# Optimization experiments

Measured on AMD Instinct MI355X. Metric: run time of the kernel, lower is better.

Reference implementation:

```python
import jax, jax.numpy as jnp
import numpy as np

# dims
B, L, IN_SIZE = 8, 4096, 1024
D_MODEL = 256            # hidden_size1
D_INNER = 512            # expand * d_model
D_STATE = 16             # mamba-ssm default
D_CONV = 4               # mamba-ssm default
DT_RANK = 16             # ceil(d_model / 16)
NUM_CLASSES = 2


def setup_inputs() -> dict:
    key = jax.random.key(0)
    ks = jax.random.split(key, 14)
    rn = lambda k, shape, s=0.02: jax.random.normal(k, shape, jnp.float32) * s
    inp = {
        "x": jax.random.normal(ks[0], (B, L, IN_SIZE), jnp.float32),
        "fc1_w": rn(ks[1], (D_MODEL, IN_SIZE)),
        "fc1_b": jnp.zeros((D_MODEL,), jnp.float32),
        "in_proj_w": rn(ks[2], (2 * D_INNER, D_MODEL)),
        "conv_w": rn(ks[3], (D_INNER, D_CONV), 0.1),
        "conv_b": jnp.zeros((D_INNER,), jnp.float32),
        "x_proj_w": rn(ks[4], (DT_RANK + 2 * D_STATE, D_INNER)),
        "dt_proj_w": rn(ks[5], (D_INNER, DT_RANK), 0.1),
        "dt_proj_b": jax.random.uniform(ks[6], (D_INNER,), jnp.float32, -4.0, -2.0),
        "A_log": jnp.tile(jnp.log(jnp.arange(1, D_STATE + 1, dtype=jnp.float32)), (D_INNER, 1)),
        "D_skip": jnp.ones((D_INNER,), jnp.float32),
        "out_proj_w": rn(ks[7], (D_MODEL, D_INNER)),
        "fc3_w": rn(ks[8], (NUM_CLASSES, D_MODEL)),
        "fc3_b": jnp.zeros((NUM_CLASSES,), jnp.float32),
    }
    return inp


def _mamba(h, in_proj_w, conv_w, conv_b, x_proj_w, dt_proj_w, dt_proj_b, A_log, D_skip, out_proj_w):
    # h: (B, L, D_MODEL)
    xz = jnp.einsum('bld,ed->ble', h, in_proj_w)          # (B, L, 2*D_INNER)
    u, z = jnp.split(xz, 2, axis=-1)                      # (B, L, D_INNER) each

    # depthwise causal conv1d along L
    uc = jnp.swapaxes(u, 1, 2)                            # (B, D_INNER, L)
    kw = conv_w[:, None, :]                               # (D_INNER, 1, K)
    uc = jax.lax.conv_general_dilated(
        uc, kw, window_strides=(1,), padding=[(D_CONV - 1, 0)],
        feature_group_count=D_INNER, dimension_numbers=('NCH', 'OIH', 'NCH'))
    uc = jax.nn.silu(uc + conv_b[None, :, None])
    u = jnp.swapaxes(uc, 1, 2)                            # (B, L, D_INNER)

    x_dbl = jnp.einsum('bld,ed->ble', u, x_proj_w)        # (B, L, DT_RANK+2*D_STATE)
    dt = x_dbl[..., :DT_RANK]
    Bmat = x_dbl[..., DT_RANK:DT_RANK + D_STATE]          # (B, L, D_STATE)
    Cmat = x_dbl[..., DT_RANK + D_STATE:]                 # (B, L, D_STATE)
    dt = jax.nn.softplus(jnp.einsum('blr,dr->bld', dt, dt_proj_w) + dt_proj_b)

    A = -jnp.exp(A_log)                                   # (D_INNER, D_STATE)

    def step(hstate, inp):
        dt_t, B_t, C_t, u_t = inp                         # (B,D),(B,S),(B,S),(B,D)
        dA = jnp.exp(dt_t[:, :, None] * A)                # (B, D, S)
        hstate = dA * hstate + (dt_t * u_t)[:, :, None] * B_t[:, None, :]
        y_t = jnp.einsum('bds,bs->bd', hstate, C_t)
        return hstate, y_t

    xs = (jnp.swapaxes(dt, 0, 1), jnp.swapaxes(Bmat, 0, 1),
          jnp.swapaxes(Cmat, 0, 1), jnp.swapaxes(u, 0, 1))
    h0 = jnp.zeros((u.shape[0], D_INNER, D_STATE), u.dtype)
    _, ys = jax.lax.scan(step, h0, xs)                    # ys: (L, B, D_INNER)
    y = jnp.swapaxes(ys, 0, 1) + u * D_skip               # (B, L, D_INNER)
    y = y * jax.nn.silu(z)
    return jnp.einsum('bld,ed->ble', y, out_proj_w)       # (B, L, D_MODEL)


def reference(x, fc1_w, fc1_b, in_proj_w, conv_w, conv_b, x_proj_w,
              dt_proj_w, dt_proj_b, A_log, D_skip, out_proj_w, fc3_w, fc3_b):
    h = jax.nn.gelu(jnp.einsum('bli,hi->blh', x, fc1_w) + fc1_b, approximate=False)
    h = _mamba(h, in_proj_w, conv_w, conv_b, x_proj_w, dt_proj_w,
               dt_proj_b, A_log, D_skip, out_proj_w)
    pooled = h.mean(axis=1)                               # (B, D_MODEL)
    return pooled @ fc3_w.T + fc3_b                       # (B, NUM_CLASSES)
```

## Files before the change

kernel.cpp:

```cpp
#include <hip/hip_runtime.h>
#include <math.h>

#define BB 8
#define LL 4096
#define BL (BB*LL)
#define IN_SZ 1024
#define D_MODEL 256
#define D_INNER 512
#define D_STATE 16
#define DT_RANK 16
#define NCLS 2
#define NCHUNK 64
#define CLEN (LL/NCHUNK)

#define OFF_XB16  ((size_t)0)
#define OFF_HB    (OFF_XB16 + (size_t)BL*1024*2)
#define OFF_XZB   (OFF_HB   + (size_t)BL*256*2)
#define OFF_UCB   (OFF_XZB  + (size_t)BL*1024*2)
#define OFF_YB    (OFF_UCB  + (size_t)BL*512*2)
#define OFF_DT    (OFF_YB   + (size_t)BL*512*2)
#define OFF_XBC   (OFF_DT   + (size_t)BL*512*4)
#define OFF_HLOC  (OFF_XBC  + (size_t)BL*32*4)
#define OFF_PP    (OFF_HLOC + (size_t)BB*NCHUNK*16*512*4)
#define OFF_H2    (OFF_PP   + (size_t)BB*NCHUNK*16*512*4)
#define OFF_WCAT  (OFF_H2   + (size_t)BL*256*4)
#define OFF_FC1WB (OFF_WCAT + (size_t)544*512*2)
#define OFF_IPWB  (OFF_FC1WB+ (size_t)256*1024*2)
#define OFF_OPWB  (OFF_IPWB + (size_t)1024*256*2)
#define OFF_POOL  (OFF_OPWB + (size_t)256*512*2)

typedef __bf16 bf16x8 __attribute__((ext_vector_type(8)));
typedef float  f32x4  __attribute__((ext_vector_type(4)));

__device__ __forceinline__ unsigned short f2bf(float f) {
    union { float f; unsigned u; } v; v.f = f;
    unsigned r = (v.u + 0x7fffu + ((v.u >> 16) & 1u)) >> 16;
    return (unsigned short)r;
}
__device__ __forceinline__ int pack2(float lo, float hi) {
    return (int)((unsigned)f2bf(lo) | ((unsigned)f2bf(hi) << 16));
}
__device__ __forceinline__ float b2f(unsigned short u) {
    union { unsigned u; float f; } v; v.u = (unsigned)u << 16; return v.f;
}
__device__ __forceinline__ float fexp(float x) { return __expf(x); }

#define GLOAD16(g, l) __builtin_amdgcn_global_load_lds( \
    (const __attribute__((address_space(1))) void*)(g), \
    (__attribute__((address_space(3))) void*)(l), 16, 0, 0)

template<int EPI, bool BOUND, int OUTBF>
__global__ __launch_bounds__(256) void gemm_bf16(
    const unsigned short* __restrict__ A, int lda,
    const unsigned short* __restrict__ Bw, int ldb,
    void* __restrict__ Cout, int ldc,
    float* __restrict__ C2,
    const float* __restrict__ bias,
    int N, int K)
{
    __shared__ unsigned short smem[2 * 128 * 64];

    const int tid  = threadIdx.x;
    const int m0   = blockIdx.y * 128;
    const int n0   = blockIdx.x * 128;
    const int wv   = tid >> 6;
    const int lane = tid & 63;
    const int wr   = wv >> 1;
    const int wc   = wv & 1;
    const int r0   = lane & 15;
    const int kgf  = lane >> 4;

    f32x4 acc[4][4];
#pragma unroll
    for (int i = 0; i < 4; i++)
#pragma unroll
        for (int j = 0; j < 4; j++) acc[i][j] = (f32x4){0.f, 0.f, 0.f, 0.f};

    for (int k0 = 0; k0 < K; k0 += 64) {
        __syncthreads();
#pragma unroll
        for (int r = 0; r < 4; r++) {
            int q   = r * 4 + wv;
            int row = q * 8 + (lane >> 3);
            int c   = (lane & 7) ^ (row & 7);
            const unsigned short* ga = A + (size_t)(m0 + row) * lda + k0 + c * 8;
            GLOAD16(ga, &smem[q * 512]);
            int nn = n0 + row;
            if (BOUND && nn > N - 1) nn = N - 1;
            const unsigned short* gb = Bw + (size_t)nn * ldb + k0 + c * 8;
            GLOAD16(gb, &smem[8192 + q * 512]);
        }
        __syncthreads();

#pragma unroll
        for (int kk = 0; kk < 2; kk++) {
            bf16x8 af[4], bfq[4];
            const int sl = ((kk << 2) + kgf) ^ (r0 & 7);
#pragma unroll
            for (int mi = 0; mi < 4; mi++)
                af[mi] = *reinterpret_cast<const bf16x8*>(
                    &smem[(wr * 64 + mi * 16 + r0) * 64 + sl * 8]);
#pragma unroll
            for (int ni = 0; ni < 4; ni++)
                bfq[ni] = *reinterpret_cast<const bf16x8*>(
                    &smem[8192 + (wc * 64 + ni * 16 + r0) * 64 + sl * 8]);
#pragma unroll
            for (int mi = 0; mi < 4; mi++)
#pragma unroll
                for (int ni = 0; ni < 4; ni++)
                    acc[mi][ni] = __builtin_amdgcn_mfma_f32_16x16x32_bf16(
                        af[mi], bfq[ni], acc[mi][ni], 0, 0, 0);
        }
    }

#pragma unroll
    for (int mi = 0; mi < 4; mi++) {
#pragma unroll
        for (int ni = 0; ni < 4; ni++) {
            int col = n0 + wc * 64 + ni * 16 + r0;
            if (BOUND && col >= N) continue;
#pragma unroll
            for (int j = 0; j < 4; j++) {
                int row = m0 + wr * 64 + mi * 16 + kgf * 4 + j;
                float v = acc[mi][ni][j];
                if (EPI == 1) {
                    v += bias[col];
                    v = 0.5f * v * (1.0f + erff(v * 0.70710678118654752f));
                } else if (EPI == 2) {
                    v += bias[col];
                    v = fmaxf(v, 0.f) + log1pf(fexp(-fabsf(v)));
                }
                if (EPI == 3) {
                    if (col < 512) {
                        v += bias[col];
                        v = fmaxf(v, 0.f) + log1pf(fexp(-fabsf(v)));
                        ((float*)Cout)[(size_t)row * 512 + col] = v;
                    } else {
                        C2[(size_t)row * 32 + (col - 512)] = v;
                    }
                } else if (OUTBF) {
                    ((unsigned short*)Cout)[(size_t)row * ldc + col] = f2bf(v);
                } else {
                    ((float*)Cout)[(size_t)row * ldc + col] = v;
                }
            }
        }
    }
}

__global__ __launch_bounds__(256) void f2b_kernel(
    const float* __restrict__ src, unsigned short* __restrict__ dst, int n8)
{
    int i = blockIdx.x * 256 + threadIdx.x;
    if (i >= n8) return;
    const float4* s = reinterpret_cast<const float4*>(src) + (size_t)i * 2;
    float4 a = s[0], b = s[1];
    int4 o;
    o.x = pack2(a.x, a.y); o.y = pack2(a.z, a.w);
    o.z = pack2(b.x, b.y); o.w = pack2(b.z, b.w);
    reinterpret_cast<int4*>(dst)[i] = o;
}

__global__ __launch_bounds__(256) void wcat_kernel(
    const float* __restrict__ dtw, const float* __restrict__ xpw,
    unsigned short* __restrict__ wcat)
{
    int idx = blockIdx.x * 256 + threadIdx.x;
    int d = idx & 511;
    int e = idx >> 9;
    float s;
    if (e < 512) {
        s = 0.f;
#pragma unroll
        for (int r = 0; r < 16; r++)
            s = fmaf(dtw[e * 16 + r], xpw[r * 512 + d], s);
    } else {
        s = xpw[(16 + e - 512) * 512 + d];
    }
    wcat[idx] = f2bf(s);
}

__global__ __launch_bounds__(256) void conv_silu(
    const unsigned short* __restrict__ xzb, const float* __restrict__ cw,
    const float* __restrict__ cb, unsigned short* __restrict__ ucb)
{
    int idx = blockIdx.x * 256 + threadIdx.x;
    if (idx >= BL * D_INNER) return;
    int d  = idx & (D_INNER - 1);
    int bl = idx >> 9;
    int l  = bl & (LL - 1);
    const float w0 = cw[d * 4 + 0], w1 = cw[d * 4 + 1];
    const float w2 = cw[d * 4 + 2], w3 = cw[d * 4 + 3];
    const unsigned short* up = xzb + (size_t)bl * 1024 + d;
    float s = cb[d];
    s = fmaf(b2f(up[0]), w3, s);
    if (l >= 1) s = fmaf(b2f(up[-1024]), w2, s);
    if (l >= 2) s = fmaf(b2f(up[-2048]), w1, s);
    if (l >= 3) s = fmaf(b2f(up[-3072]), w0, s);
    s = s / (1.f + fexp(-s));
    ucb[idx] = f2bf(s);
}

__global__ __launch_bounds__(256) void scan_pass1(
    const float* __restrict__ dtb, const unsigned short* __restrict__ ucb,
    const float* __restrict__ xbc, const float* __restrict__ A_log,
    float* __restrict__ hloc, float* __restrict__ Pp)
{
    int d = blockIdx.x * 256 + threadIdx.x;
    int c = blockIdx.y;
    int b = blockIdx.z;
    float Ac[16];
#pragma unroll
    for (int s = 0; s < 16; s++) Ac[s] = -fexp(A_log[d * 16 + s]);
    float h[16];
#pragma unroll
    for (int s = 0; s < 16; s++) h[s] = 0.f;
    float sdt = 0.f;
    int base = b * LL + c * CLEN;
    for (int t = 0; t < CLEN; t++) {
        int row = base + t;
        float dt = dtb[(size_t)row * 512 + d];
        float u  = b2f(ucb[(size_t)row * 512 + d]);
        float du = dt * u;
        sdt += dt;
        const float4* xb = reinterpret_cast<const float4*>(xbc + (size_t)row * 32);
        float Bv[16];
        float4 q;
        q = xb[0]; Bv[0]=q.x; Bv[1]=q.y; Bv[2]=q.z; Bv[3]=q.w;
        q = xb[1]; Bv[4]=q.x; Bv[5]=q.y; Bv[6]=q.z; Bv[7]=q.w;
        q = xb[2]; Bv[8]=q.x; Bv[9]=q.y; Bv[10]=q.z; Bv[11]=q.w;
        q = xb[3]; Bv[12]=q.x; Bv[13]=q.y; Bv[14]=q.z; Bv[15]=q.w;
#pragma unroll
        for (int s = 0; s < 16; s++) {
            float a = fexp(dt * Ac[s]);
            h[s] = fmaf(a, h[s], du * Bv[s]);
        }
    }
    size_t o = ((size_t)(b * NCHUNK + c) * 16) * 512 + d;
#pragma unroll
    for (int s = 0; s < 16; s++) {
        hloc[o + (size_t)s * 512] = h[s];
        Pp[o + (size_t)s * 512] = fexp(Ac[s] * sdt);
    }
}

__global__ __launch_bounds__(256) void scan_fixup(
    float* __restrict__ hloc, const float* __restrict__ Pp)
{
    int flat = blockIdx.x * 256 + threadIdx.x;
    int d  = flat & 511;
    int bs = flat >> 9;
    int b  = bs >> 4;
    int s  = bs & 15;
    float H = 0.f;
    for (int c = 0; c < NCHUNK; c++) {
        size_t idx = ((size_t)(b * NCHUNK + c) * 16 + s) * 512 + d;
        float hl = hloc[idx];
        float p  = Pp[idx];
        hloc[idx] = H;
        H = fmaf(p, H, hl);
    }
}

__global__ __launch_bounds__(256) void scan_pass2(
    const float* __restrict__ dtb, const unsigned short* __restrict__ ucb,
    const float* __restrict__ xbc, const unsigned short* __restrict__ xzb,
    const float* __restrict__ A_log, const float* __restrict__ Dskip,
    const float* __restrict__ hinit, unsigned short* __restrict__ yb)
{
    int d = blockIdx.x * 256 + threadIdx.x;
    int c = blockIdx.y;
    int b = blockIdx.z;
    float Ac[16];
#pragma unroll
    for (int s = 0; s < 16; s++) Ac[s] = -fexp(A_log[d * 16 + s]);
    float h[16];
    size_t o = ((size_t)(b * NCHUNK + c) * 16) * 512 + d;
#pragma unroll
    for (int s = 0; s < 16; s++) h[s] = hinit[o + (size_t)s * 512];
    const float Dsk = Dskip[d];
    int base = b * LL + c * CLEN;
    for (int t = 0; t < CLEN; t++) {
        int row = base + t;
        float dt = dtb[(size_t)row * 512 + d];
        float u  = b2f(ucb[(size_t)row * 512 + d]);
        float du = dt * u;
        const float4* xb = reinterpret_cast<const float4*>(xbc + (size_t)row * 32);
        float Bv[16], Cv[16];
        float4 q;
        q = xb[0]; Bv[0]=q.x; Bv[1]=q.y; Bv[2]=q.z; Bv[3]=q.w;
        q = xb[1]; Bv[4]=q.x; Bv[5]=q.y; Bv[6]=q.z; Bv[7]=q.w;
        q = xb[2]; Bv[8]=q.x; Bv[9]=q.y; Bv[10]=q.z; Bv[11]=q.w;
        q = xb[3]; Bv[12]=q.x; Bv[13]=q.y; Bv[14]=q.z; Bv[15]=q.w;
        q = xb[4]; Cv[0]=q.x; Cv[1]=q.y; Cv[2]=q.z; Cv[3]=q.w;
        q = xb[5]; Cv[4]=q.x; Cv[5]=q.y; Cv[6]=q.z; Cv[7]=q.w;
        q = xb[6]; Cv[8]=q.x; Cv[9]=q.y; Cv[10]=q.z; Cv[11]=q.w;
        q = xb[7]; Cv[12]=q.x; Cv[13]=q.y; Cv[14]=q.z; Cv[15]=q.w;
        float y = 0.f;
#pragma unroll
        for (int s = 0; s < 16; s++) {
            float a = fexp(dt * Ac[s]);
            h[s] = fmaf(a, h[s], du * Bv[s]);
            y = fmaf(h[s], Cv[s], y);
        }
        float z = b2f(xzb[(size_t)row * 1024 + 512 + d]);
        float sz = z / (1.f + fexp(-z));
        yb[(size_t)row * 512 + d] = f2bf((y + u * Dsk) * sz);
    }
}

__global__ __launch_bounds__(256) void pool_partial(
    const float* __restrict__ h2, float* __restrict__ pooled)
{
    int t = threadIdx.x;
    int chunk = blockIdx.x;
    int b = blockIdx.y;
    int l0 = chunk * (LL / 16);
    float s = 0.f;
    for (int l = l0; l < l0 + LL / 16; l++)
        s += h2[((size_t)b * LL + l) * D_MODEL + t];
    atomicAdd(&pooled[b * D_MODEL + t], s);
}

__global__ __launch_bounds__(256) void fc3_kernel(
    const float* __restrict__ pooled, const float* __restrict__ w,
    const float* __restrict__ bias, float* __restrict__ out)
{
    __shared__ float red[256];
    int t = threadIdx.x;
    int b = blockIdx.x;
    float p = pooled[b * D_MODEL + t] * (1.0f / LL);
    for (int c = 0; c < NCLS; c++) {
        red[t] = p * w[c * D_MODEL + t];
        __syncthreads();
        for (int off = 128; off > 0; off >>= 1) {
            if (t < off) red[t] += red[t + off];
            __syncthreads();
        }
        if (t == 0) out[b * NCLS + c] = red[0] + bias[c];
        __syncthreads();
    }
}

extern "C" void kernel_launch(void* const* d_in, const int* in_sizes, int n_in,
                              void* d_out, int out_size, void* d_ws, size_t ws_size,
                              hipStream_t stream)
{
    const float* x         = (const float*)d_in[0];
    const float* fc1_w     = (const float*)d_in[1];
    const float* fc1_b     = (const float*)d_in[2];
    const float* in_proj_w = (const float*)d_in[3];
    const float* conv_w    = (const float*)d_in[4];
    const float* conv_b    = (const float*)d_in[5];
    const float* x_proj_w  = (const float*)d_in[6];
    const float* dt_proj_w = (const float*)d_in[7];
    const float* dt_proj_b = (const float*)d_in[8];
    const float* A_log     = (const float*)d_in[9];
    const float* D_skip    = (const float*)d_in[10];
    const float* out_proj_w= (const float*)d_in[11];
    const float* fc3_w     = (const float*)d_in[12];
    const float* fc3_b     = (const float*)d_in[13];
    float* out = (float*)d_out;

    char* WS = (char*)d_ws;
    unsigned short* xb16  = (unsigned short*)(WS + OFF_XB16);
    unsigned short* hb    = (unsigned short*)(WS + OFF_HB);
    unsigned short* xzb   = (unsigned short*)(WS + OFF_XZB);
    unsigned short* ucb   = (unsigned short*)(WS + OFF_UCB);
    unsigned short* yb    = (unsigned short*)(WS + OFF_YB);
    float*          dtb   = (float*)(WS + OFF_DT);
    float*          xbc   = (float*)(WS + OFF_XBC);
    float*          hloc  = (float*)(WS + OFF_HLOC);
    float*          Pp    = (float*)(WS + OFF_PP);
    float*          h2    = (float*)(WS + OFF_H2);
    unsigned short* wcat  = (unsigned short*)(WS + OFF_WCAT);
    unsigned short* fc1wb = (unsigned short*)(WS + OFF_FC1WB);
    unsigned short* ipwb  = (unsigned short*)(WS + OFF_IPWB);
    unsigned short* opwb  = (unsigned short*)(WS + OFF_OPWB);
    float*          pooled= (float*)(WS + OFF_POOL);

    f2b_kernel<<<(BL * 1024 / 8) / 256, 256, 0, stream>>>(x, xb16, BL * 1024 / 8);
    f2b_kernel<<<(256 * 1024 / 8) / 256, 256, 0, stream>>>(fc1_w, fc1wb, 256 * 1024 / 8);
    f2b_kernel<<<(1024 * 256 / 8) / 256, 256, 0, stream>>>(in_proj_w, ipwb, 1024 * 256 / 8);
    f2b_kernel<<<(256 * 512 / 8) / 256, 256, 0, stream>>>(out_proj_w, opwb, 256 * 512 / 8);
    wcat_kernel<<<(544 * 512) / 256, 256, 0, stream>>>(dt_proj_w, x_proj_w, wcat);

    gemm_bf16<1, false, 1><<<dim3(2, 256), 256, 0, stream>>>(
        xb16, IN_SZ, fc1wb, IN_SZ, hb, D_MODEL, nullptr, fc1_b, D_MODEL, IN_SZ);
    gemm_bf16<0, false, 1><<<dim3(8, 256), 256, 0, stream>>>(
        hb, D_MODEL, ipwb, D_MODEL, xzb, 1024, nullptr, nullptr, 1024, D_MODEL);
    conv_silu<<<(BL * D_INNER) / 256, 256, 0, stream>>>(xzb, conv_w, conv_b, ucb);
    gemm_bf16<3, true, 0><<<dim3(5, 256), 256, 0, stream>>>(
        ucb, D_INNER, wcat, D_INNER, dtb, 512, xbc, dt_proj_b, 544, D_INNER);
    scan_pass1<<<dim3(2, NCHUNK, BB), 256, 0, stream>>>(dtb, ucb, xbc, A_log, hloc, Pp);
    scan_fixup<<<256, 256, 0, stream>>>(hloc, Pp);
    scan_pass2<<<dim3(2, NCHUNK, BB), 256, 0, stream>>>(dtb, ucb, xbc, xzb, A_log, D_skip, hloc, yb);
    gemm_bf16<0, false, 0><<<dim3(2, 256), 256, 0, stream>>>(
        yb, D_INNER, opwb, D_INNER, h2, D_MODEL, nullptr, nullptr, D_MODEL, D_INNER);
    hipMemsetAsync(pooled, 0, BB * D_MODEL * sizeof(float), stream);
    pool_partial<<<dim3(16, BB), 256, 0, stream>>>(h2, pooled);
    fc3_kernel<<<BB, 256, 0, stream>>>(pooled, fc3_w, fc3_b, out);
}
```

Before: 653.2 us.

## Double-buffer GEMM LDS tiles, swap grid axes, use fast log in softplus

The bf16 MFMA GEMM now keeps two LDS buffers. It issues the global-to-LDS loads for the next K tile before running the MFMAs on the current one, so each iteration needs one barrier instead of two. Global load pointers are computed once before the loop. The launch grid is transposed so the M tiles run along blockIdx.x, which changes the order in which blocks visit the A and B tiles and so their cache reuse. Softplus now uses __logf(1+exp) instead of log1pf, trading a little accuracy for a cheaper epilogue. The cost is double the LDS per block (64 KiB), which may reduce how many blocks fit on each CU.

```diff
diff --git a/kernel.cpp b/kernel.cpp
--- a/kernel.cpp
+++ b/kernel.cpp
@@ -58,11 +58,11 @@
     const float* __restrict__ bias,
     int N, int K)
 {
-    __shared__ unsigned short smem[2 * 128 * 64];
+    __shared__ unsigned short smem[2][16384];
 
     const int tid  = threadIdx.x;
-    const int m0   = blockIdx.y * 128;
-    const int n0   = blockIdx.x * 128;
+    const int m0   = blockIdx.x * 128;
+    const int n0   = blockIdx.y * 128;
     const int wv   = tid >> 6;
     const int lane = tid & 63;
     const int wr   = wv >> 1;
@@ -70,28 +70,45 @@
     const int r0   = lane & 15;
     const int kgf  = lane >> 4;
 
+    const unsigned short* Ag[4];
+    const unsigned short* Bg[4];
+    int ldso[4];
+#pragma unroll
+    for (int r = 0; r < 4; r++) {
+        int q   = r * 4 + wv;
+        int row = q * 8 + (lane >> 3);
+        int c   = (lane & 7) ^ (row & 7);
+        Ag[r] = A + (size_t)(m0 + row) * lda + c * 8;
+        int nn = n0 + row;
+        if (BOUND && nn > N - 1) nn = N - 1;
+        Bg[r] = Bw + (size_t)nn * ldb + c * 8;
+        ldso[r] = q * 512;
+    }
+
     f32x4 acc[4][4];
 #pragma unroll
     for (int i = 0; i < 4; i++)
 #pragma unroll
         for (int j = 0; j < 4; j++) acc[i][j] = (f32x4){0.f, 0.f, 0.f, 0.f};
 
-    for (int k0 = 0; k0 < K; k0 += 64) {
-        __syncthreads();
-#pragma unroll
-        for (int r = 0; r < 4; r++) {
-            int q   = r * 4 + wv;
-            int row = q * 8 + (lane >> 3);
-            int c   = (lane & 7) ^ (row & 7);
-            const unsigned short* ga = A + (size_t)(m0 + row) * lda + k0 + c * 8;
-            GLOAD16(ga, &smem[q * 512]);
-            int nn = n0 + row;
-            if (BOUND && nn > N - 1) nn = N - 1;
-            const unsigned short* gb = Bw + (size_t)nn * ldb + k0 + c * 8;
-            GLOAD16(gb, &smem[8192 + q * 512]);
-        }
-        __syncthreads();
-
+#pragma unroll
+    for (int r = 0; r < 4; r++) {
+        GLOAD16(Ag[r], &smem[0][ldso[r]]);
+        GLOAD16(Bg[r], &smem[0][8192 + ldso[r]]);
+    }
+    __syncthreads();
+
+    const int nk = K >> 6;
+    int cur = 0;
+    for (int t = 0; t < nk; ++t) {
+        if (t + 1 < nk) {
+            int koff = (t + 1) << 6;
+#pragma unroll
+            for (int r = 0; r < 4; r++) {
+                GLOAD16(Ag[r] + koff, &smem[cur ^ 1][ldso[r]]);
+                GLOAD16(Bg[r] + koff, &smem[cur ^ 1][8192 + ldso[r]]);
+            }
+        }
 #pragma unroll
         for (int kk = 0; kk < 2; kk++) {
             bf16x8 af[4], bfq[4];
@@ -99,11 +116,11 @@
 #pragma unroll
             for (int mi = 0; mi < 4; mi++)
                 af[mi] = *reinterpret_cast<const bf16x8*>(
-                    &smem[(wr * 64 + mi * 16 + r0) * 64 + sl * 8]);
+                    &smem[cur][(wr * 64 + mi * 16 + r0) * 64 + sl * 8]);
 #pragma unroll
             for (int ni = 0; ni < 4; ni++)
                 bfq[ni] = *reinterpret_cast<const bf16x8*>(
-                    &smem[8192 + (wc * 64 + ni * 16 + r0) * 64 + sl * 8]);
+                    &smem[cur][8192 + (wc * 64 + ni * 16 + r0) * 64 + sl * 8]);
 #pragma unroll
             for (int mi = 0; mi < 4; mi++)
 #pragma unroll
@@ -111,6 +128,8 @@
                     acc[mi][ni] = __builtin_amdgcn_mfma_f32_16x16x32_bf16(
                         af[mi], bfq[ni], acc[mi][ni], 0, 0, 0);
         }
+        __syncthreads();
+        cur ^= 1;
     }
 
 #pragma unroll
@@ -128,12 +147,12 @@
                     v = 0.5f * v * (1.0f + erff(v * 0.70710678118654752f));
                 } else if (EPI == 2) {
                     v += bias[col];
-                    v = fmaxf(v, 0.f) + log1pf(fexp(-fabsf(v)));
+                    v = fmaxf(v, 0.f) + __logf(1.f + fexp(-fabsf(v)));
                 }
                 if (EPI == 3) {
                     if (col < 512) {
                         v += bias[col];
-                        v = fmaxf(v, 0.f) + log1pf(fexp(-fabsf(v)));
+                        v = fmaxf(v, 0.f) + __logf(1.f + fexp(-fabsf(v)));
                         ((float*)Cout)[(size_t)row * 512 + col] = v;
                     } else {
                         C2[(size_t)row * 32 + (col - 512)] = v;
@@ -385,17 +404,17 @@
     f2b_kernel<<<(256 * 512 / 8) / 256, 256, 0, stream>>>(out_proj_w, opwb, 256 * 512 / 8);
     wcat_kernel<<<(544 * 512) / 256, 256, 0, stream>>>(dt_proj_w, x_proj_w, wcat);
 
-    gemm_bf16<1, false, 1><<<dim3(2, 256), 256, 0, stream>>>(
+    gemm_bf16<1, false, 1><<<dim3(256, 2), 256, 0, stream>>>(
         xb16, IN_SZ, fc1wb, IN_SZ, hb, D_MODEL, nullptr, fc1_b, D_MODEL, IN_SZ);
-    gemm_bf16<0, false, 1><<<dim3(8, 256), 256, 0, stream>>>(
+    gemm_bf16<0, false, 1><<<dim3(256, 8), 256, 0, stream>>>(
         hb, D_MODEL, ipwb, D_MODEL, xzb, 1024, nullptr, nullptr, 1024, D_MODEL);
     conv_silu<<<(BL * D_INNER) / 256, 256, 0, stream>>>(xzb, conv_w, conv_b, ucb);
-    gemm_bf16<3, true, 0><<<dim3(5, 256), 256, 0, stream>>>(
+    gemm_bf16<3, true, 0><<<dim3(256, 5), 256, 0, stream>>>(
         ucb, D_INNER, wcat, D_INNER, dtb, 512, xbc, dt_proj_b, 544, D_INNER);
     scan_pass1<<<dim3(2, NCHUNK, BB), 256, 0, stream>>>(dtb, ucb, xbc, A_log, hloc, Pp);
     scan_fixup<<<256, 256, 0, stream>>>(hloc, Pp);
     scan_pass2<<<dim3(2, NCHUNK, BB), 256, 0, stream>>>(dtb, ucb, xbc, xzb, A_log, D_skip, hloc, yb);
-    gemm_bf16<0, false, 0><<<dim3(2, 256), 256, 0, stream>>>(
+    gemm_bf16<0, false, 0><<<dim3(256, 2), 256, 0, stream>>>(
         yb, D_INNER, opwb, D_INNER, h2, D_MODEL, nullptr, nullptr, D_MODEL, D_INNER);
     hipMemsetAsync(pooled, 0, BB * D_MODEL * sizeof(float), stream);
     pool_partial<<<dim3(16, BB), 256, 0, stream>>>(h2, pooled);
```

Result: faster. 585.7 us (-10.3%).
